# Optimization experiments

Hardware: AMD Instinct MI355X
Metric: run time of the kernel (lower is better)

The kernel has to match this reference:

```python
import math
import jax, jax.numpy as jnp
import numpy as np

K = 16  # self.k from init


def knn(x, x2, k):
    # x: [B, d, P], x2: [B, d, S] -> nearest-neighbor indices [B, k, S]
    # (indices into P, per query column of x2). Matches torch knn: topk of
    # negative squared distance along dim=-2.
    x = jax.lax.stop_gradient(x)
    x2 = jax.lax.stop_gradient(x2)
    inner = -2.0 * jnp.einsum('bdp,bds->bps', x, x2)            # [B, P, S]
    xx = jnp.sum(x * x, axis=1)[:, :, None]                      # [B, P, 1]
    xx2 = jnp.sum(x2 * x2, axis=1)[:, None, :]                   # [B, 1, S]
    pd = -xx - inner - xx2                                       # [B, P, S]
    # top-k over the P axis -> move P to last axis for lax.top_k
    _, idx = jax.lax.top_k(jnp.transpose(pd, (0, 2, 1)), k)     # [B, S, k]
    return jnp.transpose(idx, (0, 2, 1))                         # [B, k, S]


def gather_neighbour(X, idx):
    # X: [B, C, P], idx: [B, n, p] -> [B, p, n, C]
    g = jax.vmap(lambda Xb, ib: Xb[:, ib])(X, idx)               # [B, C, n, p]
    return jnp.transpose(g, (0, 3, 2, 1))


def _forward(x, s_num):
    B, C, P = x.shape
    assert s_num <= P
    length = math.ceil(math.sqrt(s_num))                         # 64
    L2 = length * length                                         # == s_num (perfect square)
    mesh = jnp.arange(length, dtype=x.dtype) / length
    m01 = jnp.tile(mesh[None, :], (length, 1)).reshape(1, 1, L2)
    m02 = jnp.tile(mesh[:, None], (1, length)).reshape(1, 1, L2)
    mesh2 = jnp.concatenate([m01, m02], axis=1)                  # [1, 2, L2]
    mesh2 = jnp.broadcast_to(mesh2, (B, 2, L2))

    point_x = x[:, :2, :]                                        # [B, 2, P]
    min_x = jnp.min(point_x, axis=2, keepdims=True)
    max_x = jnp.max(point_x, axis=2, keepdims=True)
    point_sample = mesh2 * (max_x - min_x) + min_x               # [B, 2, L2]

    idx1 = knn(point_x, point_sample, 1)                         # [B, 1, L2]
    sel = gather_neighbour(x, idx1)                              # [B, L2, 1, C]
    select_point = jnp.transpose(sel[:, :, 0, :], (0, 2, 1))     # [B, C, L2]

    idx2 = knn(x[:, :3, :], select_point[:, :3, :], K)           # [B, K, s_num]
    feature = gather_neighbour(x, idx2)                          # [B, s_num, K, C]
    return jnp.transpose(feature, (0, 3, 1, 2))                  # [B, C, s_num, K]


def setup_inputs() -> dict:
    key = jax.random.key(0)
    x = jax.random.normal(key, (8, 5, 16384), dtype=jnp.float32)
    return {"x": x, "s_num": 4096}


def reference(x, s_num):
    return _forward(x, s_num)
```

## Files before the change

### kernel.cpp

```cpp
#include <hip/hip_runtime.h>

#define P 16384
#define S 4096
#define NB 8
#define CAP 12

typedef unsigned long long u64;
typedef unsigned int u32;

#define OPAQUE(x) __asm__("" : "+v"(x))

__device__ __forceinline__ u32 pd_to_dk(float pd) {
  pd = pd + 0.0f;
  u32 b = __float_as_uint(pd);
  u32 s = (u32)((int)b >> 31);
  return b ^ (~(s | 0x80000000u));
}
__device__ __forceinline__ float dk_to_pd(u32 d) {
  u32 pb = (d & 0x80000000u) ? d : (d ^ 0x7FFFFFFFu);
  return __uint_as_float(pb);
}

__device__ __forceinline__ void insert16(u64 (&L)[16], u64 key) {
#pragma unroll
  for (int j = 15; j >= 1; --j) {
    u64 a = (L[j - 1] > key) ? L[j - 1] : key;
    L[j] = (L[j] > key) ? a : L[j];
  }
  L[0] = (L[0] > key) ? key : L[0];
}

__global__ void kminmax(const float* __restrict__ x, float* __restrict__ mm) {
  int b = blockIdx.x;
  int tid = threadIdx.x;
  const float* x0 = x + (size_t)b * 5 * P;
  const float* x1 = x0 + P;
  float mn0 = __builtin_inff(), mx0 = -__builtin_inff();
  float mn1 = __builtin_inff(), mx1 = -__builtin_inff();
  for (int i = tid; i < P; i += 256) {
    float a = x0[i];
    mn0 = fminf(mn0, a); mx0 = fmaxf(mx0, a);
    float c = x1[i];
    mn1 = fminf(mn1, c); mx1 = fmaxf(mx1, c);
  }
  __shared__ float s0[256], s1[256], s2[256], s3[256];
  s0[tid] = mn0; s1[tid] = mx0; s2[tid] = mn1; s3[tid] = mx1;
  __syncthreads();
  for (int off = 128; off > 0; off >>= 1) {
    if (tid < off) {
      s0[tid] = fminf(s0[tid], s0[tid + off]);
      s1[tid] = fmaxf(s1[tid], s1[tid + off]);
      s2[tid] = fminf(s2[tid], s2[tid + off]);
      s3[tid] = fmaxf(s3[tid], s3[tid + off]);
    }
    __syncthreads();
  }
  if (tid == 0) {
    mm[b * 4 + 0] = s0[0];
    mm[b * 4 + 1] = s1[0];
    mm[b * 4 + 2] = s2[0];
    mm[b * 4 + 3] = s3[0];
  }
}

__global__ void kprep(const float* __restrict__ x, float* __restrict__ xx2d,
                      float* __restrict__ xx3d) {
#pragma clang fp contract(off)
  int gid = blockIdx.x * 256 + threadIdx.x;
  int b = gid >> 14;
  int i = gid & (P - 1);
  const float* xs = x + (size_t)b * 5 * P;
  float x0 = xs[i], x1 = xs[P + i], x2 = xs[2 * P + i];
  float t0 = x0 * x0; OPAQUE(t0);
  float t1 = x1 * x1; OPAQUE(t1);
  float t2 = x2 * x2; OPAQUE(t2);
  float s2 = t0 + t1;
  xx2d[gid] = s2;
  xx3d[gid] = s2 + t2;
}

__global__ __launch_bounds__(256) void kidx1(const float* __restrict__ x,
                                             const float* __restrict__ mm,
                                             const float* __restrict__ xx2d,
                                             u64* __restrict__ bests) {
#pragma clang fp contract(off)
  int blk = blockIdx.x;
  int b = blk >> 7;
  int sgrp = (blk >> 1) & 63;
  int half = blk & 1;
  int w = threadIdx.x >> 6, l = threadIdx.x & 63;
  const float* xs = x + (size_t)b * 5 * P;
  const float* ys = xs + P;
  float mn0 = mm[b * 4 + 0], mx0 = mm[b * 4 + 1];
  float mn1 = mm[b * 4 + 2], mx1 = mm[b * 4 + 3];
  float m0 = (float)l * (1.0f / 64.0f);
  float m1 = (float)sgrp * (1.0f / 64.0f);
  float d0 = mx0 - mn0, d1 = mx1 - mn1;
  float p0 = m0 * d0; OPAQUE(p0);
  float q0 = p0 + mn0;
  float p1 = m1 * d1; OPAQUE(p1);
  float q1 = p1 + mn1;
  float sq0 = q0 * q0; OPAQUE(sq0);
  float sq1 = q1 * q1; OPAQUE(sq1);
  float qq = sq0 + sq1;

  int base = half * 8192 + w * 2048;
  const float4* xs4 = (const float4*)(xs + base);
  const float4* ys4 = (const float4*)(ys + base);
  const float4* ws4 = (const float4*)(xx2d + b * P + base);
  float best_pd = -__builtin_inff();
  u32 best_idx = 0;
  for (int j = 0; j < 512; ++j) {
    float4 cx = xs4[j];
    float4 cy = ys4[j];
    float4 cw = ws4[j];
    float cxa[4] = {cx.x, cx.y, cx.z, cx.w};
    float cya[4] = {cy.x, cy.y, cy.z, cy.w};
    float cwa[4] = {cw.x, cw.y, cw.z, cw.w};
#pragma unroll
    for (int t = 0; t < 4; ++t) {
      float ip = __builtin_fmaf(cya[t], q1, cxa[t] * q0);
      float a  = __builtin_fmaf(2.0f, ip, -cwa[t]);
      float pd = a - qq;
      bool bt = pd > best_pd;
      best_pd  = bt ? pd : best_pd;
      best_idx = bt ? (u32)(base + (j << 2) + t) : best_idx;
    }
  }
  u64 key = ((u64)pd_to_dk(best_pd) << 32) | best_idx;
  __shared__ u64 kb[4][64];
  kb[w][l] = key;
  __syncthreads();
  if (threadIdx.x < 64) {
    u64 m = kb[0][l];
    u64 t1 = kb[1][l]; m = (t1 < m) ? t1 : m;
    u64 t2 = kb[2][l]; m = (t2 < m) ? t2 : m;
    u64 t3 = kb[3][l]; m = (t3 < m) ? t3 : m;
    bests[(size_t)(((b * 64 + sgrp) * 2 + half) * 64 + l)] = m;
  }
}

__global__ void kq(const float* __restrict__ x, const u64* __restrict__ bests,
                   float* __restrict__ qx, float* __restrict__ qy,
                   float* __restrict__ qz) {
  int qi = blockIdx.x * 256 + threadIdx.x;
  int b = qi >> 12;
  int s = qi & 4095;
  int sgrp = s >> 6, l = s & 63;
  size_t o = (size_t)(((b * 64 + sgrp) * 2) * 64 + l);
  u64 a = bests[o];
  u64 c = bests[o + 64];
  u64 m = (c < a) ? c : a;
  u32 idx = (u32)m;
  const float* xs = x + (size_t)b * 5 * P;
  qx[qi] = xs[idx];
  qy[qi] = xs[P + idx];
  qz[qi] = xs[2 * P + idx];
}

__global__ __launch_bounds__(256) void kidx2(const float* __restrict__ x,
                                             const float* __restrict__ xx3d,
                                             const float* __restrict__ qx,
                                             const float* __restrict__ qy,
                                             const float* __restrict__ qz,
                                             float* __restrict__ out) {
#pragma clang fp contract(off)
  __shared__ u64 lists[4][64][16];
  __shared__ u64 buf[256][CAP];
  int b = blockIdx.x >> 6, sgrp = blockIdx.x & 63;
  int w = threadIdx.x >> 6, l = threadIdx.x & 63;
  int s = (sgrp << 6) + l;
  int qi = (b << 12) + s;
  float q0 = qx[qi], q1 = qy[qi], q2 = qz[qi];
  float sq0 = q0 * q0; OPAQUE(sq0);
  float sq1 = q1 * q1; OPAQUE(sq1);
  float sq2 = q2 * q2; OPAQUE(sq2);
  float qq = (sq0 + sq1) + sq2;
  const float* xs = x + (size_t)b * 5 * P;
  const float* ys = xs + P;
  const float* zs = xs + 2 * P;
  int base = w * 4096;
  const float4* xs4 = (const float4*)(xs + base);
  const float4* ys4 = (const float4*)(ys + base);
  const float4* zs4 = (const float4*)(zs + base);
  const float4* ws4 = (const float4*)(xx3d + b * P + base);

  u64 L[16];
#pragma unroll
  for (int k = 0; k < 16; ++k) L[k] = 0xFF800000FFFFFFFFull;
  float thr = -__builtin_inff();
  int cnt = 0;
  u64* bufp = buf[threadIdx.x];

  auto drain = [&]() {
    while (__any(cnt > 0)) {
      if (cnt > 0) {
        --cnt;
        u64 e = bufp[cnt];
        u64 key = ((u64)pd_to_dk(__uint_as_float((u32)(e >> 32))) << 32) | (u32)e;
        if (key < L[15]) insert16(L, key);
      }
    }
    thr = dk_to_pd((u32)(L[15] >> 32));
  };

  for (int j = 0; j < 1024; ++j) {
    float4 cx = xs4[j];
    float4 cy = ys4[j];
    float4 cz = zs4[j];
    float4 cw = ws4[j];
    float cxa[4] = {cx.x, cx.y, cx.z, cx.w};
    float cya[4] = {cy.x, cy.y, cy.z, cy.w};
    float cza[4] = {cz.x, cz.y, cz.z, cz.w};
    float cwa[4] = {cw.x, cw.y, cw.z, cw.w};
#pragma unroll
    for (int t = 0; t < 4; ++t) {
      float ip = __builtin_fmaf(cza[t], q2,
                                __builtin_fmaf(cya[t], q1, cxa[t] * q0));
      float a  = __builtin_fmaf(2.0f, ip, -cwa[t]);
      float pd = a - qq;
      if (pd >= thr) {
        bufp[cnt] = ((u64)__float_as_uint(pd) << 32) | (u32)(base + (j << 2) + t);
        ++cnt;
      }
    }
    if (__any(cnt >= CAP - 4)) drain();
  }
  drain();

#pragma unroll
  for (int k = 0; k < 16; ++k) lists[w][l][k] = L[k];
  __syncthreads();

  u64* mgf = &buf[0][0];
  if (w == 0) {
    int p0 = 0, p1 = 0, p2 = 0, p3 = 0;
    u64 h0 = lists[0][l][0], h1 = lists[1][l][0];
    u64 h2 = lists[2][l][0], h3 = lists[3][l][0];
    for (int k = 0; k < 16; ++k) {
      u64 m01 = (h0 < h1) ? h0 : h1;
      u64 m23 = (h2 < h3) ? h2 : h3;
      u64 m = (m01 < m23) ? m01 : m23;
      mgf[l * 16 + k] = m;
      if (m == h0)      { ++p0; h0 = (p0 < 16) ? lists[0][l][p0] : ~0ULL; }
      else if (m == h1) { ++p1; h1 = (p1 < 16) ? lists[1][l][p1] : ~0ULL; }
      else if (m == h2) { ++p2; h2 = (p2 < 16) ? lists[2][l][p2] : ~0ULL; }
      else              { ++p3; h3 = (p3 < 16) ? lists[3][l][p3] : ~0ULL; }
    }
  }
  __syncthreads();

  int qrow = threadIdx.x >> 2;
  int g = threadIdx.x & 3;
  int sOut = (sgrp << 6) + qrow;
  u32 i0 = (u32)mgf[qrow * 16 + g * 4 + 0];
  u32 i1 = (u32)mgf[qrow * 16 + g * 4 + 1];
  u32 i2 = (u32)mgf[qrow * 16 + g * 4 + 2];
  u32 i3 = (u32)mgf[qrow * 16 + g * 4 + 3];
#pragma unroll
  for (int c = 0; c < 5; ++c) {
    const float* xc = x + (size_t)(b * 5 + c) * P;
    float4 v;
    v.x = xc[i0]; v.y = xc[i1]; v.z = xc[i2]; v.w = xc[i3];
    float* op = out + (((size_t)(b * 5 + c) * S + sOut) << 4) + (g << 2);
    *(float4*)op = v;
  }
}

extern "C" void kernel_launch(void* const* d_in, const int* in_sizes, int n_in,
                              void* d_out, int out_size, void* d_ws, size_t ws_size,
                              hipStream_t stream) {
  const float* x = (const float*)d_in[0];
  float* out = (float*)d_out;
  char* ws = (char*)d_ws;
  float* mm   = (float*)ws;
  float* xx2d = (float*)(ws + 1024);
  float* xx3d = (float*)(ws + 1024 + 524288);
  u64*   bests= (u64*)  (ws + 1024 + 2 * 524288);
  float* qx   = (float*)(ws + 1024 + 3 * 524288);
  float* qy   = qx + NB * S;
  float* qz   = qy + NB * S;

  kminmax<<<NB, 256, 0, stream>>>(x, mm);
  kprep<<<NB * P / 256, 256, 0, stream>>>(x, xx2d, xx3d);
  kidx1<<<NB * 128, 256, 0, stream>>>(x, mm, xx2d, bests);
  kq<<<NB * S / 256, 256, 0, stream>>>(x, bests, qx, qy, qz);
  kidx2<<<NB * 64, 256, 0, stream>>>(x, xx3d, qx, qy, qz, out);
}
```

Before: 670.3 us.

## Split candidate scans across more waves and move query-norm subtraction out of inner loop

kidx1 now splits the point range into quarters instead of halves, doubling the grid, and kq reduces four partial results. kidx2 uses 512 threads (8 waves, each scanning 2048 points) with an 8-way merge, a larger padded candidate buffer, and a float2 output gather. The inner loop compares the un-subtracted value against a pre-adjusted threshold (prev2 of threshold plus qq) to drop one subtraction per candidate, recomputing exact pd only during drain. This trades a longer serial 8-way merge on one wave and more shared memory for more parallelism and a cheaper inner loop; the threshold slack aims to keep results bit-exact.

```diff
diff --git a/kernel.cpp b/kernel.cpp
--- a/kernel.cpp
+++ b/kernel.cpp
@@ -3,7 +3,7 @@
 #define P 16384
 #define S 4096
 #define NB 8
-#define CAP 12
+#define CAP 16
 
 typedef unsigned long long u64;
 typedef unsigned int u32;
@@ -19,6 +19,14 @@
 __device__ __forceinline__ float dk_to_pd(u32 d) {
   u32 pb = (d & 0x80000000u) ? d : (d ^ 0x7FFFFFFFu);
   return __uint_as_float(pb);
+}
+__device__ __forceinline__ float prev2(float v) {
+  u32 b = __float_as_uint(v);
+  if ((b & 0x7F800000u) == 0x7F800000u) return v;
+  if (v > 0.0f) b -= 2;
+  else if (v < 0.0f) b += 2;
+  else return -1e-30f;
+  return __uint_as_float(b);
 }
 
 __device__ __forceinline__ void insert16(u64 (&L)[16], u64 key) {
@@ -82,12 +90,12 @@
 __global__ __launch_bounds__(256) void kidx1(const float* __restrict__ x,
                                              const float* __restrict__ mm,
                                              const float* __restrict__ xx2d,
-                                             u64* __restrict__ bests) {
+                                             u64* __restrict__ bests1) {
 #pragma clang fp contract(off)
   int blk = blockIdx.x;
-  int b = blk >> 7;
-  int sgrp = (blk >> 1) & 63;
-  int half = blk & 1;
+  int b = blk >> 8;
+  int sgrp = (blk >> 2) & 63;
+  int qtr = blk & 3;
   int w = threadIdx.x >> 6, l = threadIdx.x & 63;
   const float* xs = x + (size_t)b * 5 * P;
   const float* ys = xs + P;
@@ -104,13 +112,13 @@
   float sq1 = q1 * q1; OPAQUE(sq1);
   float qq = sq0 + sq1;
 
-  int base = half * 8192 + w * 2048;
+  int base = qtr * 4096 + w * 1024;
   const float4* xs4 = (const float4*)(xs + base);
   const float4* ys4 = (const float4*)(ys + base);
   const float4* ws4 = (const float4*)(xx2d + b * P + base);
   float best_pd = -__builtin_inff();
   u32 best_idx = 0;
-  for (int j = 0; j < 512; ++j) {
+  for (int j = 0; j < 256; ++j) {
     float4 cx = xs4[j];
     float4 cy = ys4[j];
     float4 cw = ws4[j];
@@ -136,21 +144,23 @@
     u64 t1 = kb[1][l]; m = (t1 < m) ? t1 : m;
     u64 t2 = kb[2][l]; m = (t2 < m) ? t2 : m;
     u64 t3 = kb[3][l]; m = (t3 < m) ? t3 : m;
-    bests[(size_t)(((b * 64 + sgrp) * 2 + half) * 64 + l)] = m;
-  }
-}
-
-__global__ void kq(const float* __restrict__ x, const u64* __restrict__ bests,
+    bests1[((size_t)((b * 64 + sgrp) * 4 + qtr) << 6) + l] = m;
+  }
+}
+
+__global__ void kq(const float* __restrict__ x, const u64* __restrict__ bests1,
                    float* __restrict__ qx, float* __restrict__ qy,
                    float* __restrict__ qz) {
   int qi = blockIdx.x * 256 + threadIdx.x;
   int b = qi >> 12;
   int s = qi & 4095;
   int sgrp = s >> 6, l = s & 63;
-  size_t o = (size_t)(((b * 64 + sgrp) * 2) * 64 + l);
-  u64 a = bests[o];
-  u64 c = bests[o + 64];
-  u64 m = (c < a) ? c : a;
+  size_t o = ((size_t)((b * 64 + sgrp) * 4) << 6) + l;
+  u64 m = bests1[o];
+  u64 t;
+  t = bests1[o + 64];  m = (t < m) ? t : m;
+  t = bests1[o + 128]; m = (t < m) ? t : m;
+  t = bests1[o + 192]; m = (t < m) ? t : m;
   u32 idx = (u32)m;
   const float* xs = x + (size_t)b * 5 * P;
   qx[qi] = xs[idx];
@@ -158,15 +168,15 @@
   qz[qi] = xs[2 * P + idx];
 }
 
-__global__ __launch_bounds__(256) void kidx2(const float* __restrict__ x,
+__global__ __launch_bounds__(512) void kidx2(const float* __restrict__ x,
                                              const float* __restrict__ xx3d,
                                              const float* __restrict__ qx,
                                              const float* __restrict__ qy,
                                              const float* __restrict__ qz,
                                              float* __restrict__ out) {
 #pragma clang fp contract(off)
-  __shared__ u64 lists[4][64][16];
-  __shared__ u64 buf[256][CAP];
+  __shared__ u64 buf[512][CAP + 1];
+  __shared__ u64 mgf[64][17];
   int b = blockIdx.x >> 6, sgrp = blockIdx.x & 63;
   int w = threadIdx.x >> 6, l = threadIdx.x & 63;
   int s = (sgrp << 6) + l;
@@ -179,7 +189,7 @@
   const float* xs = x + (size_t)b * 5 * P;
   const float* ys = xs + P;
   const float* zs = xs + 2 * P;
-  int base = w * 4096;
+  int base = w * 2048;
   const float4* xs4 = (const float4*)(xs + base);
   const float4* ys4 = (const float4*)(ys + base);
   const float4* zs4 = (const float4*)(zs + base);
@@ -188,7 +198,7 @@
   u64 L[16];
 #pragma unroll
   for (int k = 0; k < 16; ++k) L[k] = 0xFF800000FFFFFFFFull;
-  float thr = -__builtin_inff();
+  float thrA = -__builtin_inff();
   int cnt = 0;
   u64* bufp = buf[threadIdx.x];
 
@@ -197,14 +207,16 @@
       if (cnt > 0) {
         --cnt;
         u64 e = bufp[cnt];
-        u64 key = ((u64)pd_to_dk(__uint_as_float((u32)(e >> 32))) << 32) | (u32)e;
+        float pd = __uint_as_float((u32)(e >> 32)) - qq;
+        u64 key = ((u64)pd_to_dk(pd) << 32) | (u32)e;
         if (key < L[15]) insert16(L, key);
       }
     }
-    thr = dk_to_pd((u32)(L[15] >> 32));
+    float tp = dk_to_pd((u32)(L[15] >> 32));
+    thrA = prev2(tp + qq);
   };
 
-  for (int j = 0; j < 1024; ++j) {
+  for (int j = 0; j < 512; ++j) {
     float4 cx = xs4[j];
     float4 cy = ys4[j];
     float4 cz = zs4[j];
@@ -218,9 +230,8 @@
       float ip = __builtin_fmaf(cza[t], q2,
                                 __builtin_fmaf(cya[t], q1, cxa[t] * q0));
       float a  = __builtin_fmaf(2.0f, ip, -cwa[t]);
-      float pd = a - qq;
-      if (pd >= thr) {
-        bufp[cnt] = ((u64)__float_as_uint(pd) << 32) | (u32)(base + (j << 2) + t);
+      if (a >= thrA) {
+        bufp[cnt] = ((u64)__float_as_uint(a) << 32) | (u32)(base + (j << 2) + t);
         ++cnt;
       }
     }
@@ -229,41 +240,50 @@
   drain();
 
 #pragma unroll
-  for (int k = 0; k < 16; ++k) lists[w][l][k] = L[k];
+  for (int k = 0; k < 16; ++k) bufp[k] = L[k];
   __syncthreads();
 
-  u64* mgf = &buf[0][0];
   if (w == 0) {
-    int p0 = 0, p1 = 0, p2 = 0, p3 = 0;
-    u64 h0 = lists[0][l][0], h1 = lists[1][l][0];
-    u64 h2 = lists[2][l][0], h3 = lists[3][l][0];
+    int p0 = 0, p1 = 0, p2 = 0, p3 = 0, p4 = 0, p5 = 0, p6 = 0, p7 = 0;
+    u64 h0 = buf[l][0],        h1 = buf[64 + l][0];
+    u64 h2 = buf[128 + l][0],  h3 = buf[192 + l][0];
+    u64 h4 = buf[256 + l][0],  h5 = buf[320 + l][0];
+    u64 h6 = buf[384 + l][0],  h7 = buf[448 + l][0];
+#define ADV(i) { ++p##i; h##i = (p##i < 16) ? buf[i * 64 + l][p##i] : ~0ULL; }
     for (int k = 0; k < 16; ++k) {
       u64 m01 = (h0 < h1) ? h0 : h1;
       u64 m23 = (h2 < h3) ? h2 : h3;
-      u64 m = (m01 < m23) ? m01 : m23;
-      mgf[l * 16 + k] = m;
-      if (m == h0)      { ++p0; h0 = (p0 < 16) ? lists[0][l][p0] : ~0ULL; }
-      else if (m == h1) { ++p1; h1 = (p1 < 16) ? lists[1][l][p1] : ~0ULL; }
-      else if (m == h2) { ++p2; h2 = (p2 < 16) ? lists[2][l][p2] : ~0ULL; }
-      else              { ++p3; h3 = (p3 < 16) ? lists[3][l][p3] : ~0ULL; }
-    }
+      u64 m45 = (h4 < h5) ? h4 : h5;
+      u64 m67 = (h6 < h7) ? h6 : h7;
+      u64 ma = (m01 < m23) ? m01 : m23;
+      u64 mb = (m45 < m67) ? m45 : m67;
+      u64 m = (ma < mb) ? ma : mb;
+      mgf[l][k] = m;
+      if      (m == h0) ADV(0)
+      else if (m == h1) ADV(1)
+      else if (m == h2) ADV(2)
+      else if (m == h3) ADV(3)
+      else if (m == h4) ADV(4)
+      else if (m == h5) ADV(5)
+      else if (m == h6) ADV(6)
+      else              ADV(7)
+    }
+#undef ADV
   }
   __syncthreads();
 
-  int qrow = threadIdx.x >> 2;
-  int g = threadIdx.x & 3;
+  int qrow = threadIdx.x >> 3;
+  int g = threadIdx.x & 7;
   int sOut = (sgrp << 6) + qrow;
-  u32 i0 = (u32)mgf[qrow * 16 + g * 4 + 0];
-  u32 i1 = (u32)mgf[qrow * 16 + g * 4 + 1];
-  u32 i2 = (u32)mgf[qrow * 16 + g * 4 + 2];
-  u32 i3 = (u32)mgf[qrow * 16 + g * 4 + 3];
+  u32 i0 = (u32)mgf[qrow][g * 2 + 0];
+  u32 i1 = (u32)mgf[qrow][g * 2 + 1];
 #pragma unroll
   for (int c = 0; c < 5; ++c) {
     const float* xc = x + (size_t)(b * 5 + c) * P;
-    float4 v;
-    v.x = xc[i0]; v.y = xc[i1]; v.z = xc[i2]; v.w = xc[i3];
-    float* op = out + (((size_t)(b * 5 + c) * S + sOut) << 4) + (g << 2);
-    *(float4*)op = v;
+    float2 v;
+    v.x = xc[i0]; v.y = xc[i1];
+    float* op = out + (((size_t)(b * 5 + c) * S + sOut) << 4) + (g << 1);
+    *(float2*)op = v;
   }
 }
 
@@ -273,17 +293,17 @@
   const float* x = (const float*)d_in[0];
   float* out = (float*)d_out;
   char* ws = (char*)d_ws;
-  float* mm   = (float*)ws;
-  float* xx2d = (float*)(ws + 1024);
-  float* xx3d = (float*)(ws + 1024 + 524288);
-  u64*   bests= (u64*)  (ws + 1024 + 2 * 524288);
-  float* qx   = (float*)(ws + 1024 + 3 * 524288);
-  float* qy   = qx + NB * S;
-  float* qz   = qy + NB * S;
+  float* mm    = (float*)ws;
+  float* xx2d  = (float*)(ws + 1024);
+  float* xx3d  = (float*)(ws + 1024 + 524288);
+  u64*   bests1= (u64*)  (ws + 1024 + 2 * 524288);
+  float* qx    = (float*)(ws + 1024 + 2 * 524288 + 1048576);
+  float* qy    = qx + NB * S;
+  float* qz    = qy + NB * S;
 
   kminmax<<<NB, 256, 0, stream>>>(x, mm);
   kprep<<<NB * P / 256, 256, 0, stream>>>(x, xx2d, xx3d);
-  kidx1<<<NB * 128, 256, 0, stream>>>(x, mm, xx2d, bests);
-  kq<<<NB * S / 256, 256, 0, stream>>>(x, bests, qx, qy, qz);
-  kidx2<<<NB * 64, 256, 0, stream>>>(x, xx3d, qx, qy, qz, out);
-}
+  kidx1<<<NB * 256, 256, 0, stream>>>(x, mm, xx2d, bests1);
+  kq<<<NB * S / 256, 256, 0, stream>>>(x, bests1, qx, qy, qz);
+  kidx2<<<NB * 64, 512, 0, stream>>>(x, xx3d, qx, qy, qz, out);
+}
```

After: 621.5 us. -7.3%, faster.
